# Performance work log

Hardware: AMD Instinct MI355X
Metric: run time of the kernel (lower is better)

The kernel has to match this reference:

```python
import jax, jax.numpy as jnp
import numpy as np

N = 4096
IN_DIM = 512
NUM_HEADS = 8
SUB_DIM = 64
ETA = 0.5
LAMBDA_SPARSE = 0.1
EDGE_PROB = 0.01


def setup_inputs() -> dict:
    key = jax.random.key(0)
    k_h, k_u, k_a = jax.random.split(key, 3)
    H = jax.random.normal(k_h, (N, IN_DIM), dtype=jnp.float32)
    # Per-head orthonormal subspace bases (QR init, as in the torch module)
    raw = jax.random.normal(k_u, (NUM_HEADS, IN_DIM, SUB_DIM), dtype=jnp.float32)
    U = jax.vmap(lambda a: jnp.linalg.qr(a)[0])(raw)  # [K, in_dim, r]
    # Binary adjacency mask with self-loops (float 0/1)
    adj = (jax.random.uniform(k_a, (N, N)) < EDGE_PROB).astype(jnp.float32)
    adj_mask = jnp.maximum(adj, jnp.eye(N, dtype=jnp.float32))
    threshold = jnp.full((IN_DIM,), LAMBDA_SPARSE, dtype=jnp.float32)
    return {"H": H, "adj_mask": adj_mask, "U": U, "threshold": threshold}


def reference(H, adj_mask, U, threshold):
    r = U.shape[-1]
    scale = jnp.asarray(r, H.dtype) ** 0.5
    # Z_k = U_k^T H^T  -> [K, r, n]
    Z = jnp.einsum('kdr,nd->krn', U, H)
    # scores[k, i, j] = Z_k[:, i] . Z_k[:, j] / sqrt(r), masked to neighbors
    scores = jnp.einsum('kri,krj->kij', Z, Z) / scale
    scores = scores + (1.0 - adj_mask) * (-1e9)
    alpha = jax.nn.softmax(scores, axis=-1)          # [K, n, n]
    # Z_agg[k, :, i] = sum_j alpha[k, i, j] * Z_k[:, j]
    Z_agg = jnp.einsum('krj,kij->kri', Z, alpha)      # [K, r, n]
    # project back and sum heads: [n, d]
    agg = jnp.einsum('kdr,kri->id', U, Z_agg)
    H_half = H + ETA * agg
    H_out = jax.nn.relu(H_half - threshold[None, :])
    # orthogonality loss: sum_{k<l} ||U_k^T U_l||_F^2
    gram = jnp.einsum('kdr,lds->klrs', U, U)
    sq = jnp.sum(gram ** 2, axis=(-1, -2))            # [K, K]
    orth_loss = 0.5 * (jnp.sum(sq) - jnp.trace(sq))
    return H_out, orth_loss
```

## Files before the change

kernel.cpp:

```cpp
#include <hip/hip_runtime.h>
#include <hip/hip_bf16.h>

#define NN   4096
#define DD   512
#define KH   8
#define RR   64
#define CAP  128

typedef unsigned short u16;
typedef unsigned int   u32;
typedef __attribute__((ext_vector_type(8))) short short8;
typedef __attribute__((ext_vector_type(4))) float f32x4;

__device__ __forceinline__ float bflo(u32 v){ union{u32 i; float f;} c; c.i = v << 16;        return c.f; }
__device__ __forceinline__ float bfhi(u32 v){ union{u32 i; float f;} c; c.i = v & 0xFFFF0000u; return c.f; }
__device__ __forceinline__ u16 f2bf(float f){ __hip_bfloat16 h = __float2bfloat16(f); return *reinterpret_cast<u16*>(&h); }

__global__ __launch_bounds__(256) void prep_scan(const float* __restrict__ H, const float* __restrict__ U,
                                                 const float* __restrict__ adj,
                                                 u16* __restrict__ Hb, u16* __restrict__ Bt1,
                                                 u16* __restrict__ Bt2,
                                                 int* __restrict__ nlist, int* __restrict__ cnt,
                                                 float* __restrict__ lossA, int* __restrict__ doneA) {
    __shared__ float tile[64][65];
    __shared__ int   list[CAP];
    __shared__ int   cntS;
    const int b = blockIdx.x, t = threadIdx.x;
    if (b < 4096) {
        const int i = b;
        if (t == 0) cntS = 0;
        __syncthreads();
        const float* arow = adj + (size_t)i * NN;
        #pragma unroll
        for (int qq = 0; qq < 4; qq++) {
            int j = (qq * 256 + t) * 4;
            float4 mv = *(const float4*)(arow + j);
            if (mv.x != 0.f) { int p = atomicAdd(&cntS, 1); if (p < CAP) list[p] = j;     }
            if (mv.y != 0.f) { int p = atomicAdd(&cntS, 1); if (p < CAP) list[p] = j + 1; }
            if (mv.z != 0.f) { int p = atomicAdd(&cntS, 1); if (p < CAP) list[p] = j + 2; }
            if (mv.w != 0.f) { int p = atomicAdd(&cntS, 1); if (p < CAP) list[p] = j + 3; }
        }
        __syncthreads();
        const int n = min(cntS, CAP);
        if (t < n) nlist[(size_t)i * CAP + t] = list[t];
        if (t == 0) cnt[i] = n;
        return;
    }
    if (b < 6144) {
        size_t id = (size_t)(b - 4096) * 256 + t;
        float4 v = *(const float4*)(H + id * 4);
        ushort4 o; o.x = f2bf(v.x); o.y = f2bf(v.y); o.z = f2bf(v.z); o.w = f2bf(v.w);
        *(ushort4*)(Hb + id * 4) = o;
        return;
    }
    if (b == 6208) { if (t == 0) { lossA[0] = 0.f; doneA[0] = 0; } return; }
    const int b2 = b - 6144;
    const int k = b2 >> 3, d0 = (b2 & 7) * 64;
    #pragma unroll
    for (int s = 0; s < 4; s++) {
        int u = t + 256 * s;
        int dd = u >> 4, rq = u & 15;
        float4 v = *(const float4*)(U + ((size_t)(k * DD + d0 + dd)) * RR + rq * 4);
        tile[dd][rq * 4 + 0] = v.x; tile[dd][rq * 4 + 1] = v.y;
        tile[dd][rq * 4 + 2] = v.z; tile[dd][rq * 4 + 3] = v.w;
    }
    __syncthreads();
    {   int r = t >> 2;
        #pragma unroll
        for (int ii = 0; ii < 16; ii++) {
            int dd = (t & 3) * 16 + ii;
            Bt1[(size_t)(k * RR + r) * DD + d0 + dd] = f2bf(tile[dd][r]);
        }
    }
    {   int dd = t >> 2, rb = (t & 3) * 16;
        #pragma unroll
        for (int ii = 0; ii < 16; ii++) {
            Bt2[(size_t)(d0 + dd) * DD + k * RR + rb + ii] = f2bf(tile[dd][rb + ii]);
        }
    }
}

__global__ __launch_bounds__(256) void zgemm_mfma(const u16* __restrict__ Hb, const u16* __restrict__ Bt1,
                                                  u16* __restrict__ Zb) {
    __shared__ short As[64][72];
    __shared__ short Bs[64][72];
    const int t = threadIdx.x;
    const int i0 = blockIdx.x * 64, n0 = blockIdx.y * 64;
    const int w = t >> 6, lane = t & 63;
    const int lm = lane & 15, lg = lane >> 4;
    f32x4 acc[4] = {};
    for (int kc = 0; kc < DD; kc += 64) {
        #pragma unroll
        for (int s = 0; s < 2; s++) {
            int c = t + 256 * s; int row = c >> 3, g = c & 7;
            *(short8*)&As[row][g * 8] = *(const short8*)(Hb  + (size_t)(i0 + row) * DD + kc + g * 8);
            *(short8*)&Bs[row][g * 8] = *(const short8*)(Bt1 + (size_t)(n0 + row) * DD + kc + g * 8);
        }
        __syncthreads();
        #pragma unroll
        for (int ks = 0; ks < 64; ks += 32) {
            short8 af = *(const short8*)&As[w * 16 + lm][ks + lg * 8];
            #pragma unroll
            for (int b = 0; b < 4; b++) {
                short8 bfr = *(const short8*)&Bs[b * 16 + lm][ks + lg * 8];
                acc[b] = __builtin_amdgcn_mfma_f32_16x16x32_bf16(af, bfr, acc[b], 0, 0, 0);
            }
        }
        __syncthreads();
    }
    #pragma unroll
    for (int b = 0; b < 4; b++)
        #pragma unroll
        for (int q = 0; q < 4; q++) {
            int row = i0 + w * 16 + lg * 4 + q;
            int col = n0 + b * 16 + lm;
            Zb[(size_t)row * DD + col] = f2bf(acc[b][q]);
        }
}

__global__ __launch_bounds__(512) void attn7(const u16* __restrict__ Zb, const int* __restrict__ nlist,
                                             const int* __restrict__ cnt, u16* __restrict__ Zaggb) {
    const int i = blockIdx.x, t = threadIdx.x;
    const int k = t >> 6, lane = t & 63;
    __shared__ int   nbrS[CAP + 16];
    __shared__ float ziS[DD];
    __shared__ u32   zbufU[KH][16][36];
    __shared__ float wS[KH][16];
    const int ci = cnt[i];
    for (int u = t; u < ci; u += 512) nbrS[u] = nlist[(size_t)i * CAP + u];
    if (t < 256) {
        u32 v = *(const u32*)(Zb + (size_t)i * DD + t * 2);
        ziS[t * 2] = bflo(v); ziS[t * 2 + 1] = bfhi(v);
    }
    __syncthreads();
    if (t < 16) nbrS[ci + t] = nbrS[0];
    __syncthreads();

    const int n = lane >> 2, q = lane & 3;
    const int half = lane >> 5, L = lane & 31;
    const float4* zi4 = (const float4*)(ziS + k * 64 + q * 16);
    float m = -3.0e38f, l = 0.f, accA = 0.f, accB = 0.f;

    for (int base = 0; base < ci; base += 16) {
        const int cact = min(16, ci - base);
        const int j = nbrS[base + n];
        const uint4* zp = (const uint4*)(Zb + (size_t)j * DD + k * 64 + q * 16);
        uint4 v0 = zp[0], v1 = zp[1];
        *(uint4*)&zbufU[k][n][q * 8]     = v0;
        *(uint4*)&zbufU[k][n][q * 8 + 4] = v1;
        float4 a0 = zi4[0], a1 = zi4[1], a2 = zi4[2], a3 = zi4[3];
        float s = bflo(v0.x)*a0.x + bfhi(v0.x)*a0.y + bflo(v0.y)*a0.z + bfhi(v0.y)*a0.w
                + bflo(v0.z)*a1.x + bfhi(v0.z)*a1.y + bflo(v0.w)*a1.z + bfhi(v0.w)*a1.w
                + bflo(v1.x)*a2.x + bfhi(v1.x)*a2.y + bflo(v1.y)*a2.z + bfhi(v1.y)*a2.w
                + bflo(v1.z)*a3.x + bfhi(v1.z)*a3.y + bflo(v1.w)*a3.z + bfhi(v1.w)*a3.w;
        s += __shfl_xor(s, 1);
        s += __shfl_xor(s, 2);
        s *= 0.125f;
        if (n >= cact) s = -3.0e38f;
        float mx = s;
        #pragma unroll
        for (int off = 4; off < 64; off <<= 1) mx = fmaxf(mx, __shfl_xor(mx, off));
        const float mnew = fmaxf(m, mx);
        const float scale = __expf(m - mnew);
        const float e = (n < cact) ? __expf(s - mnew) : 0.f;
        float se = e;
        #pragma unroll
        for (int off = 4; off < 64; off <<= 1) se += __shfl_xor(se, off);
        l = l * scale + se;
        m = mnew;
        accA *= scale; accB *= scale;
        if (q == 0) wS[k][n] = e;
        __syncthreads();
        for (int c = half; c < cact; c += 2) {
            const float wgt = wS[k][c];
            u32 z2 = zbufU[k][c][L];
            accA += wgt * bflo(z2);
            accB += wgt * bfhi(z2);
        }
        __syncthreads();
    }
    accA += __shfl_xor(accA, 32);
    accB += __shfl_xor(accB, 32);
    if (lane < 32) {
        const float inv = 1.0f / l;
        u32 o = ((u32)f2bf(accA * inv)) | (((u32)f2bf(accB * inv)) << 16);
        *(u32*)(Zaggb + (size_t)i * DD + k * 64 + 2 * L) = o;
    }
}

__global__ __launch_bounds__(256) void outgemm_mfma(const u16* __restrict__ Ab, const u16* __restrict__ Btb,
                                                    const float* __restrict__ H, const float* __restrict__ thr,
                                                    float* __restrict__ out) {
    __shared__ short As[64][72];
    __shared__ short Bs[64][72];
    const int t = threadIdx.x;
    const int i0 = blockIdx.x * 64, n0 = blockIdx.y * 64;
    const int w = t >> 6, lane = t & 63;
    const int lm = lane & 15, lg = lane >> 4;
    f32x4 acc[4] = {};
    for (int kc = 0; kc < DD; kc += 64) {
        #pragma unroll
        for (int s = 0; s < 2; s++) {
            int c = t + 256 * s; int row = c >> 3, g = c & 7;
            *(short8*)&As[row][g * 8] = *(const short8*)(Ab  + (size_t)(i0 + row) * DD + kc + g * 8);
            *(short8*)&Bs[row][g * 8] = *(const short8*)(Btb + (size_t)(n0 + row) * DD + kc + g * 8);
        }
        __syncthreads();
        #pragma unroll
        for (int ks = 0; ks < 64; ks += 32) {
            short8 af = *(const short8*)&As[w * 16 + lm][ks + lg * 8];
            #pragma unroll
            for (int b = 0; b < 4; b++) {
                short8 bfr = *(const short8*)&Bs[b * 16 + lm][ks + lg * 8];
                acc[b] = __builtin_amdgcn_mfma_f32_16x16x32_bf16(af, bfr, acc[b], 0, 0, 0);
            }
        }
        __syncthreads();
    }
    #pragma unroll
    for (int b = 0; b < 4; b++) {
        const int col = n0 + b * 16 + lm;
        const float th = thr[col];
        #pragma unroll
        for (int q = 0; q < 4; q++) {
            int row = i0 + w * 16 + lg * 4 + q;
            float h = H[(size_t)row * DD + col];
            out[(size_t)row * DD + col] = fmaxf(h + 0.5f * acc[b][q] - th, 0.f);
        }
    }
}

__global__ __launch_bounds__(256) void orth_kernel(const float* __restrict__ U, float* __restrict__ loss,
                                                   int* __restrict__ done, float* __restrict__ outLoss) {
    __shared__ float UkT[64][20];
    __shared__ float UlT[64][68];
    const int pb = blockIdx.x >> 2, strip = blockIdx.x & 3;
    int idx = pb, k = 0, lh = 1;
    #pragma unroll
    for (int kk = 0; kk < 8; kk++) {
        int c = 7 - kk;
        if (idx < c) { k = kk; lh = kk + 1 + idx; break; }
        idx -= c;
    }
    const int t = threadIdx.x;
    const int r = t & 15;
    const int s0 = (t >> 4) * 4;
    const int r0g = strip * 16;
    const float* Uk = U + (size_t)k  * DD * RR;
    const float* Ul = U + (size_t)lh * DD * RR;
    float a0 = 0.f, a1 = 0.f, a2 = 0.f, a3 = 0.f;
    for (int dc = 0; dc < DD; dc += 64) {
        {   int dd = t >> 2, rq = t & 3;
            *(float4*)&UkT[dd][rq * 4] = *(const float4*)(Uk + (size_t)(dc + dd) * RR + r0g + rq * 4);
        }
        #pragma unroll
        for (int s = 0; s < 4; s++) {
            int u = t + 256 * s;
            int dd = u >> 4, sq = u & 15;
            *(float4*)&UlT[dd][sq * 4] = *(const float4*)(Ul + (size_t)(dc + dd) * RR + sq * 4);
        }
        __syncthreads();
        #pragma unroll 4
        for (int dd = 0; dd < 64; dd++) {
            float a = UkT[dd][r];
            float4 bv = *(const float4*)&UlT[dd][s0];
            a0 += a * bv.x; a1 += a * bv.y; a2 += a * bv.z; a3 += a * bv.w;
        }
        __syncthreads();
    }
    float v = a0 * a0 + a1 * a1 + a2 * a2 + a3 * a3;
    #pragma unroll
    for (int off = 32; off; off >>= 1) v += __shfl_down(v, off, 64);
    __shared__ float red[4];
    if ((t & 63) == 0) red[t >> 6] = v;
    __syncthreads();
    if (t == 0) {
        atomicAdd(loss, red[0] + red[1] + red[2] + red[3]);
        __threadfence();
        int d = atomicAdd(done, 1);
        if (d == 111) {
            float total = atomicAdd(loss, 0.f);
            outLoss[0] = total;
        }
    }
}

extern "C" void kernel_launch(void* const* d_in, const int* in_sizes, int n_in,
                              void* d_out, int out_size, void* d_ws, size_t ws_size,
                              hipStream_t stream) {
    const float* H   = (const float*)d_in[0];
    const float* adj = (const float*)d_in[1];
    const float* U   = (const float*)d_in[2];
    const float* thr = (const float*)d_in[3];
    float* out = (float*)d_out;

    char* ws = (char*)d_ws;
    float* lossA = (float*)ws;
    int*   doneA = (int*)(ws + 64);
    u16*   Hb    = (u16*)(ws + 1024);
    u16*   Zb    = (u16*)(ws + 1024 + 4u * 1024 * 1024);
    u16*   Zaggb = (u16*)(ws + 1024 + 8u * 1024 * 1024);
    u16*   Bt1   = (u16*)(ws + 1024 + 12u * 1024 * 1024);
    u16*   Bt2   = (u16*)(ws + 1024 + 12u * 1024 * 1024 + 512u * 1024);
    int*   nlist = (int*)(ws + 1024 + 13u * 1024 * 1024);
    int*   cnt   = (int*)(ws + 1024 + 15u * 1024 * 1024 + 512u * 1024);

    prep_scan<<<6209, 256, 0, stream>>>(H, U, adj, Hb, Bt1, Bt2, nlist, cnt, lossA, doneA);
    zgemm_mfma<<<dim3(64, 8), 256, 0, stream>>>(Hb, Bt1, Zb);
    attn7<<<NN, 512, 0, stream>>>(Zb, nlist, cnt, Zaggb);
    outgemm_mfma<<<dim3(64, 8), 256, 0, stream>>>(Zaggb, Bt2, H, thr, out);
    orth_kernel<<<112, 256, 0, stream>>>(U, lossA, doneA, out + (size_t)NN * DD);
}
```

Measured before the change: 173.6 us.

## Replace block barriers with wave-local LDS fences in attention; merge output GEMM and orth-loss kernels

```diff
diff --git a/kernel.cpp b/kernel.cpp
--- a/kernel.cpp
+++ b/kernel.cpp
@@ -7,6 +7,8 @@
 #define RR   64
 #define CAP  128
 
+#define WAIT_LGKM0 0xC07F
+
 typedef unsigned short u16;
 typedef unsigned int   u32;
 typedef __attribute__((ext_vector_type(8))) short short8;
@@ -15,6 +17,12 @@
 __device__ __forceinline__ float bflo(u32 v){ union{u32 i; float f;} c; c.i = v << 16;        return c.f; }
 __device__ __forceinline__ float bfhi(u32 v){ union{u32 i; float f;} c; c.i = v & 0xFFFF0000u; return c.f; }
 __device__ __forceinline__ u16 f2bf(float f){ __hip_bfloat16 h = __float2bfloat16(f); return *reinterpret_cast<u16*>(&h); }
+
+__device__ __forceinline__ void lds_fence_wave() {
+    __builtin_amdgcn_wave_barrier();
+    __builtin_amdgcn_s_waitcnt(WAIT_LGKM0);
+    __builtin_amdgcn_wave_barrier();
+}
 
 __global__ __launch_bounds__(256) void prep_scan(const float* __restrict__ H, const float* __restrict__ U,
                                                  const float* __restrict__ adj,
@@ -118,7 +126,7 @@
         }
 }
 
-__global__ __launch_bounds__(512) void attn7(const u16* __restrict__ Zb, const int* __restrict__ nlist,
+__global__ __launch_bounds__(512) void attn8(const u16* __restrict__ Zb, const int* __restrict__ nlist,
                                              const int* __restrict__ cnt, u16* __restrict__ Zaggb) {
     const int i = blockIdx.x, t = threadIdx.x;
     const int k = t >> 6, lane = t & 63;
@@ -144,6 +152,7 @@
     for (int base = 0; base < ci; base += 16) {
         const int cact = min(16, ci - base);
         const int j = nbrS[base + n];
+        lds_fence_wave();
         const uint4* zp = (const uint4*)(Zb + (size_t)j * DD + k * 64 + q * 16);
         uint4 v0 = zp[0], v1 = zp[1];
         *(uint4*)&zbufU[k][n][q * 8]     = v0;
@@ -170,14 +179,13 @@
         m = mnew;
         accA *= scale; accB *= scale;
         if (q == 0) wS[k][n] = e;
-        __syncthreads();
+        lds_fence_wave();
         for (int c = half; c < cact; c += 2) {
             const float wgt = wS[k][c];
             u32 z2 = zbufU[k][c][L];
             accA += wgt * bflo(z2);
             accB += wgt * bfhi(z2);
         }
-        __syncthreads();
     }
     accA += __shfl_xor(accA, 32);
     accB += __shfl_xor(accB, 32);
@@ -188,53 +196,56 @@
     }
 }
 
-__global__ __launch_bounds__(256) void outgemm_mfma(const u16* __restrict__ Ab, const u16* __restrict__ Btb,
-                                                    const float* __restrict__ H, const float* __restrict__ thr,
-                                                    float* __restrict__ out) {
-    __shared__ short As[64][72];
-    __shared__ short Bs[64][72];
-    const int t = threadIdx.x;
-    const int i0 = blockIdx.x * 64, n0 = blockIdx.y * 64;
-    const int w = t >> 6, lane = t & 63;
-    const int lm = lane & 15, lg = lane >> 4;
-    f32x4 acc[4] = {};
-    for (int kc = 0; kc < DD; kc += 64) {
-        #pragma unroll
-        for (int s = 0; s < 2; s++) {
-            int c = t + 256 * s; int row = c >> 3, g = c & 7;
-            *(short8*)&As[row][g * 8] = *(const short8*)(Ab  + (size_t)(i0 + row) * DD + kc + g * 8);
-            *(short8*)&Bs[row][g * 8] = *(const short8*)(Btb + (size_t)(n0 + row) * DD + kc + g * 8);
-        }
-        __syncthreads();
-        #pragma unroll
-        for (int ks = 0; ks < 64; ks += 32) {
-            short8 af = *(const short8*)&As[w * 16 + lm][ks + lg * 8];
+struct GemmSh { short As[64][72]; short Bs[64][72]; };
+struct OrthSh { float UkT[64][20]; float UlT[64][68]; float red[4]; };
+union  TailSh { GemmSh g; OrthSh o; };
+
+__global__ __launch_bounds__(256) void out_orth(const u16* __restrict__ Ab, const u16* __restrict__ Btb,
+                                                const float* __restrict__ H, const float* __restrict__ thr,
+                                                float* __restrict__ out,
+                                                const float* __restrict__ U, float* __restrict__ loss,
+                                                int* __restrict__ done, float* __restrict__ outLoss) {
+    __shared__ TailSh sh;
+    const int b = blockIdx.x, t = threadIdx.x;
+    if (b < 512) {
+        const int i0 = (b & 63) * 64, n0 = (b >> 6) * 64;
+        const int w = t >> 6, lane = t & 63;
+        const int lm = lane & 15, lg = lane >> 4;
+        f32x4 acc[4] = {};
+        for (int kc = 0; kc < DD; kc += 64) {
             #pragma unroll
-            for (int b = 0; b < 4; b++) {
-                short8 bfr = *(const short8*)&Bs[b * 16 + lm][ks + lg * 8];
-                acc[b] = __builtin_amdgcn_mfma_f32_16x16x32_bf16(af, bfr, acc[b], 0, 0, 0);
+            for (int s = 0; s < 2; s++) {
+                int c = t + 256 * s; int row = c >> 3, g = c & 7;
+                *(short8*)&sh.g.As[row][g * 8] = *(const short8*)(Ab  + (size_t)(i0 + row) * DD + kc + g * 8);
+                *(short8*)&sh.g.Bs[row][g * 8] = *(const short8*)(Btb + (size_t)(n0 + row) * DD + kc + g * 8);
             }
-        }
-        __syncthreads();
-    }
-    #pragma unroll
-    for (int b = 0; b < 4; b++) {
-        const int col = n0 + b * 16 + lm;
-        const float th = thr[col];
-        #pragma unroll
-        for (int q = 0; q < 4; q++) {
-            int row = i0 + w * 16 + lg * 4 + q;
-            float h = H[(size_t)row * DD + col];
-            out[(size_t)row * DD + col] = fmaxf(h + 0.5f * acc[b][q] - th, 0.f);
-        }
-    }
-}
-
-__global__ __launch_bounds__(256) void orth_kernel(const float* __restrict__ U, float* __restrict__ loss,
-                                                   int* __restrict__ done, float* __restrict__ outLoss) {
-    __shared__ float UkT[64][20];
-    __shared__ float UlT[64][68];
-    const int pb = blockIdx.x >> 2, strip = blockIdx.x & 3;
+            __syncthreads();
+            #pragma unroll
+            for (int ks = 0; ks < 64; ks += 32) {
+                short8 af = *(const short8*)&sh.g.As[w * 16 + lm][ks + lg * 8];
+                #pragma unroll
+                for (int bq = 0; bq < 4; bq++) {
+                    short8 bfr = *(const short8*)&sh.g.Bs[bq * 16 + lm][ks + lg * 8];
+                    acc[bq] = __builtin_amdgcn_mfma_f32_16x16x32_bf16(af, bfr, acc[bq], 0, 0, 0);
+                }
+            }
+            __syncthreads();
+        }
+        #pragma unroll
+        for (int bq = 0; bq < 4; bq++) {
+            const int col = n0 + bq * 16 + lm;
+            const float th = thr[col];
+            #pragma unroll
+            for (int q = 0; q < 4; q++) {
+                int row = i0 + w * 16 + lg * 4 + q;
+                float h = H[(size_t)row * DD + col];
+                out[(size_t)row * DD + col] = fmaxf(h + 0.5f * acc[bq][q] - th, 0.f);
+            }
+        }
+        return;
+    }
+    const int ob = b - 512;
+    const int pb = ob >> 2, strip = ob & 3;
     int idx = pb, k = 0, lh = 1;
     #pragma unroll
     for (int kk = 0; kk < 8; kk++) {
@@ -242,7 +253,6 @@
         if (idx < c) { k = kk; lh = kk + 1 + idx; break; }
         idx -= c;
     }
-    const int t = threadIdx.x;
     const int r = t & 15;
     const int s0 = (t >> 4) * 4;
     const int r0g = strip * 16;
@@ -251,19 +261,19 @@
     float a0 = 0.f, a1 = 0.f, a2 = 0.f, a3 = 0.f;
     for (int dc = 0; dc < DD; dc += 64) {
         {   int dd = t >> 2, rq = t & 3;
-            *(float4*)&UkT[dd][rq * 4] = *(const float4*)(Uk + (size_t)(dc + dd) * RR + r0g + rq * 4);
+            *(float4*)&sh.o.UkT[dd][rq * 4] = *(const float4*)(Uk + (size_t)(dc + dd) * RR + r0g + rq * 4);
         }
         #pragma unroll
         for (int s = 0; s < 4; s++) {
             int u = t + 256 * s;
             int dd = u >> 4, sq = u & 15;
-            *(float4*)&UlT[dd][sq * 4] = *(const float4*)(Ul + (size_t)(dc + dd) * RR + sq * 4);
+            *(float4*)&sh.o.UlT[dd][sq * 4] = *(const float4*)(Ul + (size_t)(dc + dd) * RR + sq * 4);
         }
         __syncthreads();
         #pragma unroll 4
         for (int dd = 0; dd < 64; dd++) {
-            float a = UkT[dd][r];
-            float4 bv = *(const float4*)&UlT[dd][s0];
+            float a = sh.o.UkT[dd][r];
+            float4 bv = *(const float4*)&sh.o.UlT[dd][s0];
             a0 += a * bv.x; a1 += a * bv.y; a2 += a * bv.z; a3 += a * bv.w;
         }
         __syncthreads();
@@ -271,11 +281,10 @@
     float v = a0 * a0 + a1 * a1 + a2 * a2 + a3 * a3;
     #pragma unroll
     for (int off = 32; off; off >>= 1) v += __shfl_down(v, off, 64);
-    __shared__ float red[4];
-    if ((t & 63) == 0) red[t >> 6] = v;
+    if ((t & 63) == 0) sh.o.red[t >> 6] = v;
     __syncthreads();
     if (t == 0) {
-        atomicAdd(loss, red[0] + red[1] + red[2] + red[3]);
+        atomicAdd(loss, sh.o.red[0] + sh.o.red[1] + sh.o.red[2] + sh.o.red[3]);
         __threadfence();
         int d = atomicAdd(done, 1);
         if (d == 111) {
@@ -307,7 +316,7 @@
 
     prep_scan<<<6209, 256, 0, stream>>>(H, U, adj, Hb, Bt1, Bt2, nlist, cnt, lossA, doneA);
     zgemm_mfma<<<dim3(64, 8), 256, 0, stream>>>(Hb, Bt1, Zb);
-    attn7<<<NN, 512, 0, stream>>>(Zb, nlist, cnt, Zaggb);
-    outgemm_mfma<<<dim3(64, 8), 256, 0, stream>>>(Zaggb, Bt2, H, thr, out);
-    orth_kernel<<<112, 256, 0, stream>>>(U, lossA, doneA, out + (size_t)NN * DD);
-}
+    attn8<<<NN, 512, 0, stream>>>(Zb, nlist, cnt, Zaggb);
+    out_orth<<<624, 256, 0, stream>>>(Zaggb, Bt2, H, thr, out,
+                                      U, lossA, doneA, out + (size_t)NN * DD);
+}
```

After: 175.3 us. No clear change (+1.0%).
